# Kernel optimization log

Hardware: AMD Instinct MI355X
Metric: run time of the kernel (lower is better)

The kernel has to match this reference:

```python
import jax, jax.numpy as jnp
import numpy as np

NUM_CLASSES = 2
THRESHOLD = 0.5
NEGPOS_RATIO = 3
VAR0, VAR1 = 0.1, 0.2  # self.variance = [0.1, 0.2]


def point_form(priors):
    # [cx,cy,w,h] -> [xmin,ymin,xmax,ymax]
    return jnp.concatenate([priors[:, :2] - priors[:, 2:] / 2,
                            priors[:, :2] + priors[:, 2:] / 2], axis=1)


def jaccard(a, b):
    # a: [O,4], b: [P,4] point-form -> IoU [O,P]
    tl = jnp.maximum(a[:, None, :2], b[None, :, :2])
    br = jnp.minimum(a[:, None, 2:], b[None, :, 2:])
    wh = jnp.clip(br - tl, 0.0)
    inter = wh[..., 0] * wh[..., 1]
    area_a = ((a[:, 2] - a[:, 0]) * (a[:, 3] - a[:, 1]))[:, None]
    area_b = ((b[:, 2] - b[:, 0]) * (b[:, 3] - b[:, 1]))[None, :]
    return inter / (area_a + area_b - inter)


def encode(matched, priors):
    # matched: [P,4] point-form GT, priors: [P,4] center-size
    g_cxcy = ((matched[:, :2] + matched[:, 2:]) / 2 - priors[:, :2]) / (VAR0 * priors[:, 2:])
    g_wh = jnp.log((matched[:, 2:] - matched[:, :2]) / priors[:, 2:]) / VAR1
    return jnp.concatenate([g_cxcy, g_wh], axis=1)


def match_one(truths, labels, priors):
    # truths: [O,4], labels: [O], priors: [P,4]
    O = truths.shape[0]
    overlaps = jaccard(truths, point_form(priors))          # [O,P]
    best_prior_idx = jnp.argmax(overlaps, axis=1)           # [O] best prior per GT
    best_truth_overlap = jnp.max(overlaps, axis=0)          # [P]
    best_truth_idx = jnp.argmax(overlaps, axis=0)           # [P]
    # ensure each GT keeps its best prior
    best_truth_overlap = best_truth_overlap.at[best_prior_idx].set(2.0)
    best_truth_idx = best_truth_idx.at[best_prior_idx].set(jnp.arange(O))
    matches = truths[best_truth_idx]                        # [P,4]
    conf = labels[best_truth_idx].astype(jnp.int32)         # head label == 1
    conf = jnp.where(best_truth_overlap < THRESHOLD, 0, conf)
    loc = encode(matches, priors)                           # [P,4]
    return loc, conf


def setup_inputs() -> dict:
    key = jax.random.key(0)
    k1, k2, k3, k4, k5, k6 = jax.random.split(key, 6)
    B, P, O = 32, 32768, 32
    loc_data = jax.random.normal(k1, (B, P, 3), jnp.float32) * 0.1
    conf_data = jax.random.normal(k2, (B, P, 2), jnp.float32)
    cxy = jax.random.uniform(k3, (P, 2), jnp.float32, 0.1, 0.9)
    wh = jax.random.uniform(k4, (P, 2), jnp.float32, 0.05, 0.2)
    priors = jnp.concatenate([cxy, wh], axis=1)
    xy1 = jax.random.uniform(k5, (B, O, 2), jnp.float32, 0.0, 0.7)
    twh = jax.random.uniform(k6, (B, O, 2), jnp.float32, 0.05, 0.25)
    targets = jnp.concatenate([xy1, xy1 + twh, jnp.ones((B, O, 1), jnp.float32)], axis=2)
    return {"loc_data": loc_data, "conf_data": conf_data, "priors": priors, "targets": targets}


def reference(loc_data, conf_data, priors, targets):
    B, P, _ = loc_data.shape
    # convert_coord: [cx, cy, gw] -> [cx, cy, gw, gw]
    quard = jnp.stack([loc_data[..., 0], loc_data[..., 1],
                       loc_data[..., 2], loc_data[..., 2]], axis=-1)  # [B,P,4]
    truths = targets[..., :4]
    labels = targets[..., 4]
    loc_t, conf_t = jax.vmap(lambda t, l: match_one(t, l, priors))(truths, labels)
    pos = conf_t > 0                                         # [B,P]
    # localization smooth-L1 over positives (sum reduction)
    d = quard - loc_t
    ad = jnp.abs(d)
    sl1 = jnp.where(ad < 1.0, 0.5 * d * d, ad - 0.5)
    loss_l = jnp.sum(sl1 * pos[..., None].astype(sl1.dtype))
    # per-prior CE for hard-negative mining
    lse = jax.nn.logsumexp(conf_data, axis=-1)               # [B,P]
    picked = jnp.take_along_axis(conf_data, conf_t[..., None], axis=-1)[..., 0]
    ce = lse - picked                                        # [B,P]
    ce_mine = jnp.where(pos, 0.0, ce)
    # double argsort -> rank of each prior by mining loss (descending)
    loss_idx = jnp.argsort(-ce_mine, axis=1)
    idx_rank = jnp.argsort(loss_idx, axis=1)
    num_pos = jnp.sum(pos.astype(jnp.int32), axis=1, keepdims=True)  # [B,1]
    num_neg = jnp.minimum(NEGPOS_RATIO * num_pos, P - 1)
    neg = idx_rank < num_neg
    sel = jnp.logical_or(pos, neg)
    loss_c = jnp.sum(jnp.where(sel, ce, 0.0))
    N = jnp.sum(num_pos).astype(loss_l.dtype)
    return loss_l / N, loss_c / N
```

## Files before the change

### kernel.cpp

```cpp
#include <hip/hip_runtime.h>
#include <math.h>

#define Bn 32
#define Pn 32768
#define On 32
#define TPB 256
#define PPT 4
#define BP  (TPB * PPT)


__global__ __launch_bounds__(256) void matchA(const float4* __restrict__ priors,
                                              const float* __restrict__ targets,
                                              unsigned long long* __restrict__ bpm) {
    int bo = blockIdx.x, chunk = blockIdx.y;
    const float* t = targets + (size_t)bo * 5;
    float tx1 = t[0], ty1 = t[1], tx2 = t[2], ty2 = t[3];
    float area_a = (tx2 - tx1) * (ty2 - ty1);

    int base = chunk * (Pn / 4) + threadIdx.x;
    float bI[4] = {0.f, 0.f, 0.f, 0.f};
    float bU[4] = {1.f, 1.f, 1.f, 1.f};
    int   bp[4];
#pragma unroll
    for (int c = 0; c < 4; c++) bp[c] = base + 256 * c;

#pragma unroll 2
    for (int i = 0; i < 8; i++) {
#pragma unroll
        for (int c = 0; c < 4; c++) {
            int p = base + (i * 4 + c) * 256;
            float4 pr = priors[p];
            float px1 = pr.x - pr.z * 0.5f, py1 = pr.y - pr.w * 0.5f;
            float px2 = pr.x + pr.z * 0.5f, py2 = pr.y + pr.w * 0.5f;
            float ix1 = fmaxf(tx1, px1), iy1 = fmaxf(ty1, py1);
            float ix2 = fminf(tx2, px2), iy2 = fminf(ty2, py2);
            float iw = fmaxf(ix2 - ix1, 0.f), ih = fmaxf(iy2 - iy1, 0.f);
            float I = iw * ih;
            float U = area_a + (px2 - px1) * (py2 - py1) - I;
            if (I * bU[c] > bI[c] * U) { bI[c] = I; bU[c] = U; bp[c] = p; }
        }
    }
    unsigned long long key = 0ull;
#pragma unroll
    for (int c = 0; c < 4; c++) {
        float iou = bI[c] / bU[c];
        unsigned long long kc = ((unsigned long long)__float_as_uint(iou) << 32)
                              | (unsigned)(Pn - 1 - bp[c]);
        if (kc > key) key = kc;
    }

    __shared__ unsigned long long sk[256];
    sk[threadIdx.x] = key;
    __syncthreads();
    for (int s = 128; s > 0; s >>= 1) {
        if ((int)threadIdx.x < s) {
            unsigned long long o = sk[threadIdx.x + s];
            if (o > sk[threadIdx.x]) sk[threadIdx.x] = o;
        }
        __syncthreads();
    }
    if (threadIdx.x == 0) atomicMax(&bpm[bo], sk[0]);
}

__global__ __launch_bounds__(256) void matchB(const float* __restrict__ loc,
                                              const float2* __restrict__ conf2,
                                              const float4* __restrict__ priors,
                                              const float* __restrict__ targets,
                                              const unsigned long long* __restrict__ bpm,
                                              float* __restrict__ ce_mine,
                                              int* __restrict__ num_pos,
                                              float* __restrict__ loss_l_t,
                                              float* __restrict__ ce_t,
                                              int* __restrict__ np_tot) {
    int b = blockIdx.y;
    int base = blockIdx.x * BP;
    int tid = threadIdx.x;

    __shared__ float4 tb[On];
    __shared__ float  ta[On], lb[On];
    __shared__ int    forced[BP];
    __shared__ float  sred[12];

#pragma unroll
    for (int j = 0; j < PPT; j++) forced[tid + 256 * j] = -1;
    int sp = -1;
    if (tid < On) {
        const float* t = targets + ((size_t)b * On + tid) * 5;
        float x1 = t[0], y1 = t[1], x2 = t[2], y2 = t[3];
        tb[tid] = make_float4(x1, y1, x2, y2);
        ta[tid] = (x2 - x1) * (y2 - y1);
        lb[tid] = t[4];
        sp = Pn - 1 - (int)(bpm[b * On + tid] & 0xFFFFFFFFull);
    }
    __syncthreads();
    if (tid < On && sp >= base && sp < base + BP)
        atomicMax(&forced[sp - base], tid);
    __syncthreads();

    float px1[PPT], py1[PPT], px2[PPT], py2[PPT], ab[PPT], pcx[PPT], pcy[PPT], pw[PPT], ph[PPT];
#pragma unroll
    for (int j = 0; j < PPT; j++) {
        float4 pr = priors[base + tid + 256 * j];
        pcx[j] = pr.x; pcy[j] = pr.y; pw[j] = pr.z; ph[j] = pr.w;
        px1[j] = pr.x - pr.z * 0.5f; py1[j] = pr.y - pr.w * 0.5f;
        px2[j] = pr.x + pr.z * 0.5f; py2[j] = pr.y + pr.w * 0.5f;
        ab[j]  = (px2[j] - px1[j]) * (py2[j] - py1[j]);
    }

    float bI[PPT] = {0.f, 0.f, 0.f, 0.f};
    float bU[PPT] = {1.f, 1.f, 1.f, 1.f};
    int   bx[PPT] = {0, 0, 0, 0};
#pragma unroll 4
    for (int o = 0; o < On; o++) {
        float4 tt = tb[o];
        float  a  = ta[o];
#pragma unroll
        for (int j = 0; j < PPT; j++) {
            float ix1 = fmaxf(tt.x, px1[j]), iy1 = fmaxf(tt.y, py1[j]);
            float ix2 = fminf(tt.z, px2[j]), iy2 = fminf(tt.w, py2[j]);
            float iw = fmaxf(ix2 - ix1, 0.f), ih = fmaxf(iy2 - iy1, 0.f);
            float I = iw * ih;
            float U = a + ab[j] - I;
            if (I * bU[j] > bI[j] * U) { bI[j] = I; bU[j] = U; bx[j] = o; }
        }
    }

    float ll_s = 0.f, pce_s = 0.f, cnt_s = 0.f;
#pragma unroll
    for (int j = 0; j < PPT; j++) {
        int p = base + tid + 256 * j;
        int fo = forced[tid + 256 * j];
        int bidx = (fo >= 0) ? fo : bx[j];
        int cf;
        if (fo >= 0)                      cf = (int)lb[bidx];
        else if (bI[j] >= 0.5f * bU[j])   cf = (int)lb[bidx];
        else                              cf = 0;
        bool pos = cf > 0;

        if (pos) {
            float4 tt = tb[bidx];
            float g0 = ((tt.x + tt.z) * 0.5f - pcx[j]) / (0.1f * pw[j]);
            float g1 = ((tt.y + tt.w) * 0.5f - pcy[j]) / (0.1f * ph[j]);
            float g2 = __logf((tt.z - tt.x) / pw[j]) * 5.0f;
            float g3 = __logf((tt.w - tt.y) / ph[j]) * 5.0f;
            const float* lp = loc + ((size_t)b * Pn + p) * 3;
            float q0 = lp[0], q1 = lp[1], q2 = lp[2];
            float dd[4] = { q0 - g0, q1 - g1, q2 - g2, q2 - g3 };
#pragma unroll
            for (int i = 0; i < 4; i++) {
                float ad = fabsf(dd[i]);
                ll_s += (ad < 1.f) ? 0.5f * dd[i] * dd[i] : (ad - 0.5f);
            }
            cnt_s += 1.f;
        }

        float2 cc = conf2[(size_t)b * Pn + p];
        float m = fmaxf(cc.x, cc.y);
        float lse = m + __logf(__expf(cc.x - m) + __expf(cc.y - m));
        float ce = lse - (cf ? cc.y : cc.x);
        if (pos) { pce_s += ce; ce = 0.f; }
        ce_mine[(size_t)b * Pn + p] = fmaxf(ce, 0.f);
    }

#pragma unroll
    for (int off = 32; off > 0; off >>= 1) {
        ll_s  += __shfl_down(ll_s,  off, 64);
        pce_s += __shfl_down(pce_s, off, 64);
        cnt_s += __shfl_down(cnt_s, off, 64);
    }
    int lane = tid & 63, wv = tid >> 6;
    if (lane == 0) { sred[wv * 3] = ll_s; sred[wv * 3 + 1] = pce_s; sred[wv * 3 + 2] = cnt_s; }
    __syncthreads();
    if (tid == 0) {
        float llr = 0, pcer = 0, cntr = 0;
        for (int w = 0; w < 4; w++) { llr += sred[w*3]; pcer += sred[w*3+1]; cntr += sred[w*3+2]; }
        if (llr != 0.f)  atomicAdd(loss_l_t, llr);
        if (pcer != 0.f) atomicAdd(ce_t, pcer);
        int c = (int)cntr;
        if (c) { atomicAdd(&num_pos[b], c); atomicAdd(np_tot, c); }
    }
}

__global__ __launch_bounds__(1024) void topk(const float* __restrict__ ce_mine,
                                             const int* __restrict__ num_pos,
                                             float* __restrict__ ce_t) {
    int b = blockIdx.x, tid = threadIdx.x;
    const float4* v4 = (const float4*)(ce_mine + (size_t)b * Pn);
    float4 r[8];
#pragma unroll
    for (int i = 0; i < 8; i++) r[i] = v4[i * 1024 + tid];

    int k = 3 * num_pos[b];
    if (k > Pn - 1) k = Pn - 1;
    if (k <= 0) return;

    __shared__ int   scnt[16];
    __shared__ float ssum[16];
    __shared__ int   s_tot;

    unsigned lo = 0u, hi = 0x7F800000u;
    while (hi - lo > 1u) {
        unsigned mid = lo + ((hi - lo) >> 1);
        float mf = __uint_as_float(mid);
        int c = 0;
#pragma unroll
        for (int i = 0; i < 8; i++) {
            c += (r[i].x > mf) + (r[i].y > mf) + (r[i].z > mf) + (r[i].w > mf);
        }
#pragma unroll
        for (int off = 32; off > 0; off >>= 1) c += __shfl_down(c, off, 64);
        if ((tid & 63) == 0) scnt[tid >> 6] = c;
        __syncthreads();
        if (tid == 0) { int t = 0; for (int w = 0; w < 16; w++) t += scnt[w]; s_tot = t; }
        __syncthreads();
        if (s_tot >= k) lo = mid; else hi = mid;
    }
    float tv = __uint_as_float(hi);
    float s = 0.f; int c = 0;
#pragma unroll
    for (int i = 0; i < 8; i++) {
        if (r[i].x > tv) { s += r[i].x; c++; }
        if (r[i].y > tv) { s += r[i].y; c++; }
        if (r[i].z > tv) { s += r[i].z; c++; }
        if (r[i].w > tv) { s += r[i].w; c++; }
    }
#pragma unroll
    for (int off = 32; off > 0; off >>= 1) {
        s += __shfl_down(s, off, 64);
        c += __shfl_down(c, off, 64);
    }
    if ((tid & 63) == 0) { ssum[tid >> 6] = s; scnt[tid >> 6] = c; }
    __syncthreads();
    if (tid == 0) {
        float st = 0.f; int ct = 0;
        for (int w = 0; w < 16; w++) { st += ssum[w]; ct += scnt[w]; }
        atomicAdd(ce_t, st + (float)(k - ct) * tv);
    }
}

__global__ void finalize(const float* __restrict__ loss_l_t,
                         const float* __restrict__ ce_t,
                         const int* __restrict__ np_tot,
                         float* __restrict__ out) {
    float N = (float)(*np_tot);
    out[0] = *loss_l_t / N;
    out[1] = *ce_t / N;
}

extern "C" void kernel_launch(void* const* d_in, const int* in_sizes, int n_in,
                              void* d_out, int out_size, void* d_ws, size_t ws_size,
                              hipStream_t stream) {
    const float* loc     = (const float*)d_in[0];
    const float* conf    = (const float*)d_in[1];
    const float* priors  = (const float*)d_in[2];
    const float* targets = (const float*)d_in[3];
    float* out = (float*)d_out;

    char* ws = (char*)d_ws;
    unsigned long long* bpm = (unsigned long long*)ws;
    int*   num_pos  = (int*)(ws + 8192);
    float* loss_l_t = (float*)(ws + 8320);
    float* ce_t     = (float*)(ws + 8324);
    int*   np_tot   = (int*)(ws + 8328);
    float* ce_mine  = (float*)(ws + 16384);

    hipMemsetAsync(ws, 0, 16384, stream);

    hipLaunchKernelGGL(matchA, dim3(Bn * On, 4), dim3(256), 0, stream,
                       (const float4*)priors, targets, bpm);
    hipLaunchKernelGGL(matchB, dim3(Pn / BP, Bn), dim3(256), 0, stream,
                       loc, (const float2*)conf, (const float4*)priors, targets, bpm,
                       ce_mine, num_pos, loss_l_t, ce_t, np_tot);
    hipLaunchKernelGGL(topk, dim3(Bn), dim3(1024), 0, stream, ce_mine, num_pos, ce_t);
    hipLaunchKernelGGL(finalize, dim3(1), dim3(1), 0, stream, loss_l_t, ce_t, np_tot, out);
}
```

Baseline: 171.7 us.

## Compute IoU once per prior-GT pair, pack best-match results for second pass

The IoU matrix was computed twice, once per GT for best-prior and again per prior for best-truth. Now a single pass computes both: it tracks the per-prior best GT and does a per-GT wave-shuffle argmax, then writes a packed byte per prior (index plus threshold flag) for the second kernel. The second kernel reads the pack and vectorized conf loads, and writes ce_mine as float4 instead of recomputing IoU. The topk binary search drops one barrier per round by using per-round atomic counters and exits early on an exact count match. This adds a workspace buffer and per-GT shuffle reductions inside the loop.

```diff
diff --git a/kernel.cpp b/kernel.cpp
--- a/kernel.cpp
+++ b/kernel.cpp
@@ -4,146 +4,144 @@
 #define Bn 32
 #define Pn 32768
 #define On 32
-#define TPB 256
-#define PPT 4
-#define BP  (TPB * PPT)
-
-
-__global__ __launch_bounds__(256) void matchA(const float4* __restrict__ priors,
+
+
+__global__ __launch_bounds__(256) void phase1(const float4* __restrict__ priors,
                                               const float* __restrict__ targets,
-                                              unsigned long long* __restrict__ bpm) {
-    int bo = blockIdx.x, chunk = blockIdx.y;
-    const float* t = targets + (size_t)bo * 5;
-    float tx1 = t[0], ty1 = t[1], tx2 = t[2], ty2 = t[3];
-    float area_a = (tx2 - tx1) * (ty2 - ty1);
-
-    int base = chunk * (Pn / 4) + threadIdx.x;
+                                              unsigned long long* __restrict__ bpm,
+                                              uchar4* __restrict__ pack) {
+    int b = blockIdx.y;
+    int base = blockIdx.x * 1024;
+    int tid = threadIdx.x;
+    int lane = tid & 63, wv = tid >> 6;
+
+    __shared__ float4 tb[On];
+    __shared__ float  ta[On];
+    __shared__ unsigned long long wred[On][4];
+
+    if (tid < On) {
+        const float* t = targets + ((size_t)b * On + tid) * 5;
+        float x1 = t[0], y1 = t[1], x2 = t[2], y2 = t[3];
+        tb[tid] = make_float4(x1, y1, x2, y2);
+        ta[tid] = (x2 - x1) * (y2 - y1);
+    }
+    __syncthreads();
+
+    int p0 = base + tid * 4;
+    float px1[4], py1[4], px2[4], py2[4], ab[4];
+#pragma unroll
+    for (int j = 0; j < 4; j++) {
+        float4 pr = priors[p0 + j];
+        px1[j] = pr.x - pr.z * 0.5f; py1[j] = pr.y - pr.w * 0.5f;
+        px2[j] = pr.x + pr.z * 0.5f; py2[j] = pr.y + pr.w * 0.5f;
+        ab[j]  = (px2[j] - px1[j]) * (py2[j] - py1[j]);
+    }
+
     float bI[4] = {0.f, 0.f, 0.f, 0.f};
     float bU[4] = {1.f, 1.f, 1.f, 1.f};
-    int   bp[4];
-#pragma unroll
-    for (int c = 0; c < 4; c++) bp[c] = base + 256 * c;
-
-#pragma unroll 2
-    for (int i = 0; i < 8; i++) {
-#pragma unroll
-        for (int c = 0; c < 4; c++) {
-            int p = base + (i * 4 + c) * 256;
-            float4 pr = priors[p];
-            float px1 = pr.x - pr.z * 0.5f, py1 = pr.y - pr.w * 0.5f;
-            float px2 = pr.x + pr.z * 0.5f, py2 = pr.y + pr.w * 0.5f;
-            float ix1 = fmaxf(tx1, px1), iy1 = fmaxf(ty1, py1);
-            float ix2 = fminf(tx2, px2), iy2 = fminf(ty2, py2);
+    int   bx[4] = {0, 0, 0, 0};
+
+    for (int o = 0; o < On; o++) {
+        float4 tt = tb[o];
+        float  a  = ta[o];
+        float I[4], U[4];
+#pragma unroll
+        for (int j = 0; j < 4; j++) {
+            float ix1 = fmaxf(tt.x, px1[j]), iy1 = fmaxf(tt.y, py1[j]);
+            float ix2 = fminf(tt.z, px2[j]), iy2 = fminf(tt.w, py2[j]);
             float iw = fmaxf(ix2 - ix1, 0.f), ih = fmaxf(iy2 - iy1, 0.f);
-            float I = iw * ih;
-            float U = area_a + (px2 - px1) * (py2 - py1) - I;
-            if (I * bU[c] > bI[c] * U) { bI[c] = I; bU[c] = U; bp[c] = p; }
+            I[j] = iw * ih;
+            U[j] = a + ab[j] - I[j];
+            if (I[j] * bU[j] > bI[j] * U[j]) { bI[j] = I[j]; bU[j] = U[j]; bx[j] = o; }
         }
-    }
-    unsigned long long key = 0ull;
-#pragma unroll
-    for (int c = 0; c < 4; c++) {
-        float iou = bI[c] / bU[c];
-        unsigned long long kc = ((unsigned long long)__float_as_uint(iou) << 32)
-                              | (unsigned)(Pn - 1 - bp[c]);
-        if (kc > key) key = kc;
-    }
-
-    __shared__ unsigned long long sk[256];
-    sk[threadIdx.x] = key;
-    __syncthreads();
-    for (int s = 128; s > 0; s >>= 1) {
-        if ((int)threadIdx.x < s) {
-            unsigned long long o = sk[threadIdx.x + s];
-            if (o > sk[threadIdx.x]) sk[threadIdx.x] = o;
+        float cI = I[0], cU = U[0]; int cp = p0;
+#pragma unroll
+        for (int j = 1; j < 4; j++)
+            if (I[j] * cU > cI * U[j]) { cI = I[j]; cU = U[j]; cp = p0 + j; }
+        float iou = cI / cU;
+        unsigned long long key = ((unsigned long long)__float_as_uint(iou) << 32)
+                               | (unsigned)(Pn - 1 - cp);
+#pragma unroll
+        for (int off = 32; off > 0; off >>= 1) {
+            unsigned long long ok = __shfl_down(key, off, 64);
+            if (ok > key) key = ok;
         }
-        __syncthreads();
-    }
-    if (threadIdx.x == 0) atomicMax(&bpm[bo], sk[0]);
-}
-
-__global__ __launch_bounds__(256) void matchB(const float* __restrict__ loc,
-                                              const float2* __restrict__ conf2,
+        if (lane == 0) wred[o][wv] = key;
+    }
+    __syncthreads();
+    if (tid < On) {
+        unsigned long long kk = wred[tid][0];
+#pragma unroll
+        for (int w = 1; w < 4; w++) if (wred[tid][w] > kk) kk = wred[tid][w];
+        atomicMax(&bpm[b * On + tid], kk);
+    }
+
+    uchar4 pk;
+    pk.x = (unsigned char)(bx[0] | ((bI[0] >= 0.5f * bU[0]) ? 32 : 0));
+    pk.y = (unsigned char)(bx[1] | ((bI[1] >= 0.5f * bU[1]) ? 32 : 0));
+    pk.z = (unsigned char)(bx[2] | ((bI[2] >= 0.5f * bU[2]) ? 32 : 0));
+    pk.w = (unsigned char)(bx[3] | ((bI[3] >= 0.5f * bU[3]) ? 32 : 0));
+    pack[(size_t)b * (Pn / 4) + blockIdx.x * 256 + tid] = pk;
+}
+
+__global__ __launch_bounds__(256) void phase2(const float* __restrict__ loc,
+                                              const float4* __restrict__ conf4,
                                               const float4* __restrict__ priors,
                                               const float* __restrict__ targets,
                                               const unsigned long long* __restrict__ bpm,
+                                              const uchar4* __restrict__ pack,
                                               float* __restrict__ ce_mine,
                                               int* __restrict__ num_pos,
                                               float* __restrict__ loss_l_t,
                                               float* __restrict__ ce_t,
                                               int* __restrict__ np_tot) {
     int b = blockIdx.y;
-    int base = blockIdx.x * BP;
+    int base = blockIdx.x * 1024;
     int tid = threadIdx.x;
 
     __shared__ float4 tb[On];
-    __shared__ float  ta[On], lb[On];
-    __shared__ int    forced[BP];
+    __shared__ float  lb[On];
+    __shared__ int    forced[1024];
     __shared__ float  sred[12];
 
-#pragma unroll
-    for (int j = 0; j < PPT; j++) forced[tid + 256 * j] = -1;
+    forced[tid] = -1; forced[tid + 256] = -1; forced[tid + 512] = -1; forced[tid + 768] = -1;
     int sp = -1;
     if (tid < On) {
         const float* t = targets + ((size_t)b * On + tid) * 5;
-        float x1 = t[0], y1 = t[1], x2 = t[2], y2 = t[3];
-        tb[tid] = make_float4(x1, y1, x2, y2);
-        ta[tid] = (x2 - x1) * (y2 - y1);
+        tb[tid] = make_float4(t[0], t[1], t[2], t[3]);
         lb[tid] = t[4];
         sp = Pn - 1 - (int)(bpm[b * On + tid] & 0xFFFFFFFFull);
     }
     __syncthreads();
-    if (tid < On && sp >= base && sp < base + BP)
+    if (tid < On && sp >= base && sp < base + 1024)
         atomicMax(&forced[sp - base], tid);
     __syncthreads();
 
-    float px1[PPT], py1[PPT], px2[PPT], py2[PPT], ab[PPT], pcx[PPT], pcy[PPT], pw[PPT], ph[PPT];
-#pragma unroll
-    for (int j = 0; j < PPT; j++) {
-        float4 pr = priors[base + tid + 256 * j];
-        pcx[j] = pr.x; pcy[j] = pr.y; pw[j] = pr.z; ph[j] = pr.w;
-        px1[j] = pr.x - pr.z * 0.5f; py1[j] = pr.y - pr.w * 0.5f;
-        px2[j] = pr.x + pr.z * 0.5f; py2[j] = pr.y + pr.w * 0.5f;
-        ab[j]  = (px2[j] - px1[j]) * (py2[j] - py1[j]);
-    }
-
-    float bI[PPT] = {0.f, 0.f, 0.f, 0.f};
-    float bU[PPT] = {1.f, 1.f, 1.f, 1.f};
-    int   bx[PPT] = {0, 0, 0, 0};
-#pragma unroll 4
-    for (int o = 0; o < On; o++) {
-        float4 tt = tb[o];
-        float  a  = ta[o];
-#pragma unroll
-        for (int j = 0; j < PPT; j++) {
-            float ix1 = fmaxf(tt.x, px1[j]), iy1 = fmaxf(tt.y, py1[j]);
-            float ix2 = fminf(tt.z, px2[j]), iy2 = fminf(tt.w, py2[j]);
-            float iw = fmaxf(ix2 - ix1, 0.f), ih = fmaxf(iy2 - iy1, 0.f);
-            float I = iw * ih;
-            float U = a + ab[j] - I;
-            if (I * bU[j] > bI[j] * U) { bI[j] = I; bU[j] = U; bx[j] = o; }
-        }
-    }
-
+    int p0 = base + tid * 4;
+    uchar4 pk = pack[(size_t)b * (Pn / 4) + blockIdx.x * 256 + tid];
+    size_t cb = ((size_t)b * Pn + p0) >> 1;
+    float4 cA = conf4[cb], cB = conf4[cb + 1];
+
+    unsigned char pkb[4] = {pk.x, pk.y, pk.z, pk.w};
+    float c0a[4] = {cA.x, cA.z, cB.x, cB.z};
+    float c1a[4] = {cA.y, cA.w, cB.y, cB.w};
+    float cem[4];
     float ll_s = 0.f, pce_s = 0.f, cnt_s = 0.f;
-#pragma unroll
-    for (int j = 0; j < PPT; j++) {
-        int p = base + tid + 256 * j;
-        int fo = forced[tid + 256 * j];
-        int bidx = (fo >= 0) ? fo : bx[j];
-        int cf;
-        if (fo >= 0)                      cf = (int)lb[bidx];
-        else if (bI[j] >= 0.5f * bU[j])   cf = (int)lb[bidx];
-        else                              cf = 0;
+
+#pragma unroll
+    for (int j = 0; j < 4; j++) {
+        int fo = forced[tid * 4 + j];
+        int bidx = (fo >= 0) ? fo : (pkb[j] & 31);
+        int cf = ((fo >= 0) || (pkb[j] & 32)) ? (int)lb[bidx] : 0;
         bool pos = cf > 0;
-
         if (pos) {
             float4 tt = tb[bidx];
-            float g0 = ((tt.x + tt.z) * 0.5f - pcx[j]) / (0.1f * pw[j]);
-            float g1 = ((tt.y + tt.w) * 0.5f - pcy[j]) / (0.1f * ph[j]);
-            float g2 = __logf((tt.z - tt.x) / pw[j]) * 5.0f;
-            float g3 = __logf((tt.w - tt.y) / ph[j]) * 5.0f;
-            const float* lp = loc + ((size_t)b * Pn + p) * 3;
+            float4 pr = priors[p0 + j];
+            float g0 = ((tt.x + tt.z) * 0.5f - pr.x) / (0.1f * pr.z);
+            float g1 = ((tt.y + tt.w) * 0.5f - pr.y) / (0.1f * pr.w);
+            float g2 = __logf((tt.z - tt.x) / pr.z) * 5.0f;
+            float g3 = __logf((tt.w - tt.y) / pr.w) * 5.0f;
+            const float* lp = loc + ((size_t)b * Pn + p0 + j) * 3;
             float q0 = lp[0], q1 = lp[1], q2 = lp[2];
             float dd[4] = { q0 - g0, q1 - g1, q2 - g2, q2 - g3 };
 #pragma unroll
@@ -153,14 +151,13 @@
             }
             cnt_s += 1.f;
         }
-
-        float2 cc = conf2[(size_t)b * Pn + p];
-        float m = fmaxf(cc.x, cc.y);
-        float lse = m + __logf(__expf(cc.x - m) + __expf(cc.y - m));
-        float ce = lse - (cf ? cc.y : cc.x);
+        float m = fmaxf(c0a[j], c1a[j]);
+        float lse = m + __logf(__expf(c0a[j] - m) + __expf(c1a[j] - m));
+        float ce = lse - (cf ? c1a[j] : c0a[j]);
         if (pos) { pce_s += ce; ce = 0.f; }
-        ce_mine[(size_t)b * Pn + p] = fmaxf(ce, 0.f);
-    }
+        cem[j] = fmaxf(ce, 0.f);
+    }
+    ((float4*)ce_mine)[((size_t)b * Pn + p0) >> 2] = make_float4(cem[0], cem[1], cem[2], cem[3]);
 
 #pragma unroll
     for (int off = 32; off > 0; off >>= 1) {
@@ -169,7 +166,7 @@
         cnt_s += __shfl_down(cnt_s, off, 64);
     }
     int lane = tid & 63, wv = tid >> 6;
-    if (lane == 0) { sred[wv * 3] = ll_s; sred[wv * 3 + 1] = pce_s; sred[wv * 3 + 2] = cnt_s; }
+    if (lane == 0) { sred[wv*3] = ll_s; sred[wv*3+1] = pce_s; sred[wv*3+2] = cnt_s; }
     __syncthreads();
     if (tid == 0) {
         float llr = 0, pcer = 0, cntr = 0;
@@ -194,27 +191,31 @@
     if (k > Pn - 1) k = Pn - 1;
     if (k <= 0) return;
 
-    __shared__ int   scnt[16];
+    __shared__ int   scnt[34];
     __shared__ float ssum[16];
-    __shared__ int   s_tot;
+    __shared__ int   sct[16];
+    for (int i = tid; i < 34; i += 1024) scnt[i] = 0;
+    __syncthreads();
 
     unsigned lo = 0u, hi = 0x7F800000u;
-    while (hi - lo > 1u) {
+    int round = 0;
+    while (hi - lo > 1u && round < 32) {
         unsigned mid = lo + ((hi - lo) >> 1);
         float mf = __uint_as_float(mid);
         int c = 0;
 #pragma unroll
-        for (int i = 0; i < 8; i++) {
+        for (int i = 0; i < 8; i++)
             c += (r[i].x > mf) + (r[i].y > mf) + (r[i].z > mf) + (r[i].w > mf);
-        }
 #pragma unroll
         for (int off = 32; off > 0; off >>= 1) c += __shfl_down(c, off, 64);
-        if ((tid & 63) == 0) scnt[tid >> 6] = c;
+        if ((tid & 63) == 0) atomicAdd(&scnt[round], c);
         __syncthreads();
-        if (tid == 0) { int t = 0; for (int w = 0; w < 16; w++) t += scnt[w]; s_tot = t; }
-        __syncthreads();
-        if (s_tot >= k) lo = mid; else hi = mid;
-    }
+        int tot = scnt[round];
+        round++;
+        if (tot == k) { hi = mid; break; }
+        if (tot >= k) lo = mid; else hi = mid;
+    }
+
     float tv = __uint_as_float(hi);
     float s = 0.f; int c = 0;
 #pragma unroll
@@ -229,11 +230,11 @@
         s += __shfl_down(s, off, 64);
         c += __shfl_down(c, off, 64);
     }
-    if ((tid & 63) == 0) { ssum[tid >> 6] = s; scnt[tid >> 6] = c; }
+    if ((tid & 63) == 0) { ssum[tid >> 6] = s; sct[tid >> 6] = c; }
     __syncthreads();
     if (tid == 0) {
         float st = 0.f; int ct = 0;
-        for (int w = 0; w < 16; w++) { st += ssum[w]; ct += scnt[w]; }
+        for (int w = 0; w < 16; w++) { st += ssum[w]; ct += sct[w]; }
         atomicAdd(ce_t, st + (float)(k - ct) * tv);
     }
 }
@@ -262,14 +263,15 @@
     float* loss_l_t = (float*)(ws + 8320);
     float* ce_t     = (float*)(ws + 8324);
     int*   np_tot   = (int*)(ws + 8328);
-    float* ce_mine  = (float*)(ws + 16384);
+    uchar4* pack    = (uchar4*)(ws + 16384);
+    float* ce_mine  = (float*)(ws + 16384 + (size_t)Bn * Pn);
 
     hipMemsetAsync(ws, 0, 16384, stream);
 
-    hipLaunchKernelGGL(matchA, dim3(Bn * On, 4), dim3(256), 0, stream,
-                       (const float4*)priors, targets, bpm);
-    hipLaunchKernelGGL(matchB, dim3(Pn / BP, Bn), dim3(256), 0, stream,
-                       loc, (const float2*)conf, (const float4*)priors, targets, bpm,
+    hipLaunchKernelGGL(phase1, dim3(Pn / 1024, Bn), dim3(256), 0, stream,
+                       (const float4*)priors, targets, bpm, pack);
+    hipLaunchKernelGGL(phase2, dim3(Pn / 1024, Bn), dim3(256), 0, stream,
+                       loc, (const float4*)conf, (const float4*)priors, targets, bpm, pack,
                        ce_mine, num_pos, loss_l_t, ce_t, np_tot);
     hipLaunchKernelGGL(topk, dim3(Bn), dim3(1024), 0, stream, ce_mine, num_pos, ce_t);
     hipLaunchKernelGGL(finalize, dim3(1), dim3(1), 0, stream, loss_l_t, ce_t, np_tot, out);
```

Result: slower. 175.7 us (+2.3%).
